# Kernel optimization log

Hardware: AMD Instinct MI355X
Metric: run time of the kernel (lower is better)

The kernel has to match this reference:

```python
import jax, jax.numpy as jnp
import numpy as np

KERNEL_MUL = 2.0
KERNEL_NUM = 5


def setup_inputs() -> dict:
    key = jax.random.key(0)
    k1, k2 = jax.random.split(key)
    source = jax.random.normal(k1, (4096, 256), dtype=jnp.float32)
    target = jax.random.normal(k2, (4096, 256), dtype=jnp.float32)
    return {"source": source, "target": target}


def _mmd(source, target):
    n = source.shape[0]
    m = target.shape[0]
    ns = n + m
    total = jnp.concatenate([source, target], axis=0)  # [ns, D]
    # Pairwise squared L2 distances without the O(ns^2 * D) broadcast tensor:
    # ||x_i - x_j||^2 = ||x_i||^2 + ||x_j||^2 - 2 <x_i, x_j>
    sq = jnp.sum(total * total, axis=1)  # [ns]
    l2 = sq[:, None] + sq[None, :] - 2.0 * (total @ total.T)  # [ns, ns]
    # bandwidth computed on detached data in the original (L2_distance.data)
    bandwidth = jax.lax.stop_gradient(jnp.sum(l2)) / (ns * ns - ns)
    bandwidth = bandwidth / (KERNEL_MUL ** (KERNEL_NUM // 2))
    # multi-bandwidth Gaussian kernel sum (fused single pass over l2)
    kernels = jnp.zeros_like(l2)
    for i in range(KERNEL_NUM):
        kernels = kernels + jnp.exp(-l2 / (bandwidth * KERNEL_MUL ** i))
    xx = jnp.sum(kernels[:n, :n]) / (n * n)
    xy = jnp.sum(kernels[:n, n:]) / (-n * m)
    yx = jnp.sum(kernels[n:, :n]) / (-m * n)
    yy = jnp.sum(kernels[n:, n:]) / (m * m)
    return xx + xy + yx + yy


def reference(source, target):
    return _mmd(source, target)
```

## Files before the change

### kernel.cpp

```cpp
#include <hip/hip_runtime.h>
#include <hip/hip_bf16.h>
#include <stdint.h>

#define NS 8192
#define NHALF 4096
#define DIM 256
#define BLK 128
#define BK 32
#define NKT (DIM / BK)
#define NTILES (NS / BLK)
#define HALF_TILES (NHALF / BLK)
#define NTRI (NTILES * (NTILES + 1) / 2)
#define PREP_BLOCKS 256

typedef __attribute__((ext_vector_type(8))) short bf16x8;
typedef __attribute__((ext_vector_type(4))) float f32x4;
typedef __attribute__((ext_vector_type(2))) float f32x2;
typedef __attribute__((ext_vector_type(8))) unsigned short u16x8;

#define XB_OFF   0
#define SQ_OFF   (NS * DIM * 2)
#define PART_OFF (SQ_OFF + NS * 4)
#define ACC_OFF  (PART_OFF + PREP_BLOCKS * DIM * 4)
#define C0_OFF   (ACC_OFF + 8)
#define WS_NEED  (C0_OFF + 16)

__device__ __forceinline__ unsigned short f2bf(float f) {
  unsigned int u = __float_as_uint(f);
  u += 0x7fffu + ((u >> 16) & 1u);
  return (unsigned short)(u >> 16);
}
__device__ __forceinline__ float bf2f(unsigned short h) {
  return __uint_as_float(((unsigned int)h) << 16);
}

__device__ __forceinline__ float fast_exp2(float x) {
#if __has_builtin(__builtin_amdgcn_exp2f)
  return __builtin_amdgcn_exp2f(x);
#else
  return exp2f(x);
#endif
}

__global__ __launch_bounds__(256) void mmd_prep(
    const float* __restrict__ src, const float* __restrict__ tgt,
    unsigned short* __restrict__ Xb, float* __restrict__ sq,
    float* __restrict__ partials, double* __restrict__ accK) {
  int tid = threadIdx.x;
  if (blockIdx.x == 0 && tid == 0) accK[0] = 0.0;
  int lane32 = tid & 31;
  int rgrp = tid >> 5;
  int c = lane32 * 8;
  int rowBase = blockIdx.x * 32;

  float colpart[8];
#pragma unroll
  for (int j = 0; j < 8; ++j) colpart[j] = 0.f;

#pragma unroll
  for (int p = 0; p < 4; ++p) {
    int row = rowBase + p * 8 + rgrp;
    const float* X = (row < NHALF) ? (src + (size_t)row * DIM)
                                   : (tgt + (size_t)(row - NHALF) * DIM);
    float4 v0 = *(const float4*)(X + c);
    float4 v1 = *(const float4*)(X + c + 4);
    float vals[8] = {v0.x, v0.y, v0.z, v0.w, v1.x, v1.y, v1.z, v1.w};
    u16x8 h;
    float s = 0.f;
#pragma unroll
    for (int j = 0; j < 8; ++j) {
      unsigned short b = f2bf(vals[j]);
      h[j] = b;
      float rb = bf2f(b);
      s += rb * rb;
      colpart[j] += rb;
    }
    *(u16x8*)(Xb + (size_t)row * DIM + c) = h;
    for (int o = 16; o > 0; o >>= 1) s += __shfl_down(s, o, 32);
    if (lane32 == 0) sq[row] = s;
  }

  __shared__ float cp[8][DIM];
  *(float4*)&cp[rgrp][c]     = make_float4(colpart[0], colpart[1], colpart[2], colpart[3]);
  *(float4*)&cp[rgrp][c + 4] = make_float4(colpart[4], colpart[5], colpart[6], colpart[7]);
  __syncthreads();
  float s8 = 0.f;
#pragma unroll
  for (int r = 0; r < 8; ++r) s8 += cp[r][tid];
  partials[blockIdx.x * DIM + tid] = s8;
}

__global__ __launch_bounds__(1024) void mmd_band(
    const float* __restrict__ partials, const float* __restrict__ sq,
    float* __restrict__ c0out) {
  __shared__ float CS[4][DIM];
  __shared__ float L1[1024];
  __shared__ double D2[DIM];
  int tid = threadIdx.x;
  int q = tid >> 8, col = tid & 255;
  float cs = 0.f;
  for (int b = 0; b < PREP_BLOCKS / 4; ++b)
    cs += partials[(q * 64 + b) * DIM + col];
  CS[q][col] = cs;
  const float4* s4 = (const float4*)sq;
  float4 va = s4[tid * 2], vb = s4[tid * 2 + 1];
  L1[tid] = (va.x + va.y + va.z + va.w) + (vb.x + vb.y + vb.z + vb.w);
  __syncthreads();
  if (tid < DIM) {
    float ctot = (CS[0][tid] + CS[1][tid]) + (CS[2][tid] + CS[3][tid]);
    D2[tid] = (double)ctot * (double)ctot;
    L1[tid] = (L1[tid] + L1[tid + 256]) + (L1[tid + 512] + L1[tid + 768]);
  }
  __syncthreads();
  for (int o = 128; o > 0; o >>= 1) {
    if (tid < o) { D2[tid] += D2[tid + o]; L1[tid] += L1[tid + o]; }
    __syncthreads();
  }
  if (tid == 0) {
    double S1 = (double)L1[0];
    double S2 = D2[0];
    double sum_l2 = 2.0 * (double)NS * S1 - 2.0 * S2;
    double bw = sum_l2 / ((double)NS * (double)NS - (double)NS);
    bw = bw / 4.0;
    c0out[0] = (float)(1.4426950408889634 / bw);
  }
}

#define STAGE(KT, BUF)                                                        \
  {                                                                           \
    _Pragma("unroll") for (int it = 0; it < 2; ++it) {                        \
      int idx = it * 256 + tid;                         \
      int r = idx >> 2, g = idx & 3;          \
      int gs = g ^ ((r >> 1) & 3);          \
      const unsigned short* ga =                                              \
          Xb + (size_t)(rowBase + r) * DIM + (KT)*BK + gs * 8;                \
      __builtin_amdgcn_global_load_lds(                                       \
          (const __attribute__((address_space(1))) void*)ga,                  \
          (__attribute__((address_space(3))) void*)(&As[BUF][idx * 8]), 16,   \
          0, 0);                                                              \
      const unsigned short* gb =                                              \
          Xb + (size_t)(colBase + r) * DIM + (KT)*BK + gs * 8;                \
      __builtin_amdgcn_global_load_lds(                                       \
          (const __attribute__((address_space(1))) void*)gb,                  \
          (__attribute__((address_space(3))) void*)(&Bs[BUF][idx * 8]), 16,   \
          0, 0);                                                              \
    }                                                                         \
  }

__global__ __launch_bounds__(256, 2) void mmd_gram(
    const unsigned short* __restrict__ Xb, const float* __restrict__ sq,
    const float* __restrict__ c0p, double* __restrict__ accK) {
  int l = blockIdx.x;
  int bj = (int)((sqrtf(8.f * (float)l + 1.f) - 1.f) * 0.5f);
  while ((bj + 1) * (bj + 2) / 2 <= l) bj++;
  while (bj * (bj + 1) / 2 > l) bj--;
  int bi = l - bj * (bj + 1) / 2;

  __shared__ __align__(16) unsigned short As[3][BLK * BK];
  __shared__ __align__(16) unsigned short Bs[3][BLK * BK];
  int tid = threadIdx.x;
  int wave = tid >> 6;
  int lane = tid & 63;
  int rowBase = bi * BLK, colBase = bj * BLK;
  int wr = (wave >> 1) * 64;
  int wc = (wave & 1) * 64;

  float c0v = *c0p;
  int r4 = (lane >> 4) * 4;
  f32x4 sqr4[4];
#pragma unroll
  for (int m = 0; m < 4; ++m)
    sqr4[m] = *(const f32x4*)&sq[rowBase + wr + m * 16 + r4];
  float sqc[4];
#pragma unroll
  for (int n = 0; n < 4; ++n)
    sqc[n] = sq[colBase + wc + n * 16 + (lane & 15)];

  f32x4 acc[4][4];
#pragma unroll
  for (int m = 0; m < 4; ++m)
#pragma unroll
    for (int n = 0; n < 4; ++n) acc[m][n] = (f32x4){0.f, 0.f, 0.f, 0.f};

  STAGE(0, 0);
  STAGE(1, 1);

#pragma unroll
  for (int kt = 0; kt < NKT; ++kt) {
    int cur = kt % 3;
    if (kt == NKT - 1)
      asm volatile("s_waitcnt vmcnt(0)" ::: "memory");
    else
      asm volatile("s_waitcnt vmcnt(4)" ::: "memory");
    __builtin_amdgcn_s_barrier();
    __builtin_amdgcn_sched_barrier(0);

    bf16x8 af[4], bfr[4];
    int kg = lane >> 4;
#pragma unroll
    for (int m = 0; m < 4; ++m) {
      int r = wr + m * 16 + (lane & 15);
      af[m] = *(const bf16x8*)(&As[cur][r * BK + (kg ^ ((r >> 1) & 3)) * 8]);
    }
#pragma unroll
    for (int n = 0; n < 4; ++n) {
      int r = wc + n * 16 + (lane & 15);
      bfr[n] = *(const bf16x8*)(&Bs[cur][r * BK + (kg ^ ((r >> 1) & 3)) * 8]);
    }

    if (kt < NKT - 2) STAGE(kt + 2, (kt + 2) % 3);

#pragma unroll
    for (int m = 0; m < 4; ++m)
#pragma unroll
      for (int n = 0; n < 4; ++n)
        acc[m][n] = __builtin_amdgcn_mfma_f32_16x16x32_bf16(
            af[m], bfr[n], acc[m][n], 0, 0, 0);
  }

  float cE = -0.0625f * c0v;
  float t2 = -2.f * cE;
  f32x2 t2v = (f32x2){t2, t2};
  f32x2 aP[4][2];
#pragma unroll
  for (int m = 0; m < 4; ++m)
#pragma unroll
    for (int p = 0; p < 2; ++p)
      aP[m][p] = (f32x2){cE * sqr4[m][p * 2], cE * sqr4[m][p * 2 + 1]};
  f32x2 ts = (f32x2){0.f, 0.f};
#pragma unroll
  for (int m = 0; m < 4; ++m)
#pragma unroll
    for (int n = 0; n < 4; ++n) {
      f32x2 bv = (f32x2){cE * sqc[n], cE * sqc[n]};
#pragma unroll
      for (int p = 0; p < 2; ++p) {
        f32x2 a2 = (f32x2){acc[m][n][p * 2], acc[m][n][p * 2 + 1]};
        f32x2 arg = a2 * t2v + (aP[m][p] + bv);
        f32x2 e4;
        e4.x = fast_exp2(arg.x);
        e4.y = fast_exp2(arg.y);
        f32x2 e3 = e4 * e4;
        f32x2 e2 = e3 * e3;
        f32x2 e1 = e2 * e2;
        f32x2 e0 = e1 * e1;
        ts += ((e4 + e3) + (e2 + e1)) + e0;
      }
    }
  float tsum = ts.x + ts.y;

  float* red4 = (float*)&As[0][0];
#pragma unroll
  for (int o = 32; o > 0; o >>= 1) tsum += __shfl_down(tsum, o);
  if (lane == 0) red4[wave] = tsum;
  __syncthreads();
  if (tid == 0) {
    float t = (red4[0] + red4[1]) + (red4[2] + red4[3]);
    float sign = ((bi < HALF_TILES) == (bj < HALF_TILES)) ? 1.f : -1.f;
    float factor = (bi == bj) ? sign : 2.f * sign;
    atomicAdd(accK, (double)(factor * t));
  }
}

__global__ void mmd_final(const double* __restrict__ accK, float* __restrict__ out) {
  out[0] = (float)(accK[0] / ((double)NHALF * (double)NHALF));
}

extern "C" void kernel_launch(void* const* d_in, const int* in_sizes, int n_in,
                              void* d_out, int out_size, void* d_ws, size_t ws_size,
                              hipStream_t stream) {
  if (ws_size < (size_t)WS_NEED) return;
  const float* src = (const float*)d_in[0];
  const float* tgt = (const float*)d_in[1];
  char* ws = (char*)d_ws;
  unsigned short* Xb = (unsigned short*)(ws + XB_OFF);
  float* sq          = (float*)(ws + SQ_OFF);
  float* partials    = (float*)(ws + PART_OFF);
  double* accK       = (double*)(ws + ACC_OFF);
  float* c0          = (float*)(ws + C0_OFF);

  mmd_prep<<<PREP_BLOCKS, 256, 0, stream>>>(src, tgt, Xb, sq, partials, accK);
  mmd_band<<<1, 1024, 0, stream>>>(partials, sq, c0);
  mmd_gram<<<NTRI, 256, 0, stream>>>(Xb, sq, c0, accK);
  mmd_final<<<1, 1, 0, stream>>>(accK, (float*)d_out);
}
```

Baseline: 56.37 us.

## Eliminate bandwidth reduction kernel via atomics and recompute bandwidth per gram block

The separate single-block bandwidth kernel is removed. The prep kernel now atomically accumulates column sums and the total squared-norm sum into zeroed workspace, and every gram block recomputes the bandwidth from those 256 column sums with a wave reduction. Gram block indices are remapped with a stride-8 interleave, and the next-stage global-to-LDS prefetch is issued before the LDS fragment reads. This drops one serial launch and its tail latency, at the cost of a memset launch, float atomics whose summation order is nondeterministic, and redundant per-block bandwidth math.

Result: slower. 93.02 us (+65.0%).

```diff
diff --git a/kernel.cpp b/kernel.cpp
--- a/kernel.cpp
+++ b/kernel.cpp
@@ -20,10 +20,11 @@
 
 #define XB_OFF   0
 #define SQ_OFF   (NS * DIM * 2)
-#define PART_OFF (SQ_OFF + NS * 4)
-#define ACC_OFF  (PART_OFF + PREP_BLOCKS * DIM * 4)
-#define C0_OFF   (ACC_OFF + 8)
-#define WS_NEED  (C0_OFF + 16)
+#define ACC_OFF  (SQ_OFF + NS * 4)
+#define S1_OFF   (ACC_OFF + 8)
+#define CS_OFF   (ACC_OFF + 16)
+#define ZERO_BYTES (16 + DIM * 4)
+#define WS_NEED  (CS_OFF + DIM * 4)
 
 __device__ __forceinline__ unsigned short f2bf(float f) {
   unsigned int u = __float_as_uint(f);
@@ -45,9 +46,8 @@
 __global__ __launch_bounds__(256) void mmd_prep(
     const float* __restrict__ src, const float* __restrict__ tgt,
     unsigned short* __restrict__ Xb, float* __restrict__ sq,
-    float* __restrict__ partials, double* __restrict__ accK) {
+    float* __restrict__ colsum, float* __restrict__ S1p) {
   int tid = threadIdx.x;
-  if (blockIdx.x == 0 && tid == 0) accK[0] = 0.0;
   int lane32 = tid & 31;
   int rgrp = tid >> 5;
   int c = lane32 * 8;
@@ -56,6 +56,7 @@
   float colpart[8];
 #pragma unroll
   for (int j = 0; j < 8; ++j) colpart[j] = 0.f;
+  float ssum = 0.f;
 
 #pragma unroll
   for (int p = 0; p < 4; ++p) {
@@ -77,52 +78,24 @@
     }
     *(u16x8*)(Xb + (size_t)row * DIM + c) = h;
     for (int o = 16; o > 0; o >>= 1) s += __shfl_down(s, o, 32);
-    if (lane32 == 0) sq[row] = s;
+    if (lane32 == 0) { sq[row] = s; ssum += s; }
   }
 
   __shared__ float cp[8][DIM];
+  __shared__ float rowsum[8];
   *(float4*)&cp[rgrp][c]     = make_float4(colpart[0], colpart[1], colpart[2], colpart[3]);
   *(float4*)&cp[rgrp][c + 4] = make_float4(colpart[4], colpart[5], colpart[6], colpart[7]);
+  if (lane32 == 0) rowsum[rgrp] = ssum;
   __syncthreads();
   float s8 = 0.f;
 #pragma unroll
   for (int r = 0; r < 8; ++r) s8 += cp[r][tid];
-  partials[blockIdx.x * DIM + tid] = s8;
-}
-
-__global__ __launch_bounds__(1024) void mmd_band(
-    const float* __restrict__ partials, const float* __restrict__ sq,
-    float* __restrict__ c0out) {
-  __shared__ float CS[4][DIM];
-  __shared__ float L1[1024];
-  __shared__ double D2[DIM];
-  int tid = threadIdx.x;
-  int q = tid >> 8, col = tid & 255;
-  float cs = 0.f;
-  for (int b = 0; b < PREP_BLOCKS / 4; ++b)
-    cs += partials[(q * 64 + b) * DIM + col];
-  CS[q][col] = cs;
-  const float4* s4 = (const float4*)sq;
-  float4 va = s4[tid * 2], vb = s4[tid * 2 + 1];
-  L1[tid] = (va.x + va.y + va.z + va.w) + (vb.x + vb.y + vb.z + vb.w);
-  __syncthreads();
-  if (tid < DIM) {
-    float ctot = (CS[0][tid] + CS[1][tid]) + (CS[2][tid] + CS[3][tid]);
-    D2[tid] = (double)ctot * (double)ctot;
-    L1[tid] = (L1[tid] + L1[tid + 256]) + (L1[tid + 512] + L1[tid + 768]);
-  }
-  __syncthreads();
-  for (int o = 128; o > 0; o >>= 1) {
-    if (tid < o) { D2[tid] += D2[tid + o]; L1[tid] += L1[tid + o]; }
-    __syncthreads();
-  }
+  atomicAdd(&colsum[tid], s8);
   if (tid == 0) {
-    double S1 = (double)L1[0];
-    double S2 = D2[0];
-    double sum_l2 = 2.0 * (double)NS * S1 - 2.0 * S2;
-    double bw = sum_l2 / ((double)NS * (double)NS - (double)NS);
-    bw = bw / 4.0;
-    c0out[0] = (float)(1.4426950408889634 / bw);
+    float t = 0.f;
+#pragma unroll
+    for (int r = 0; r < 8; ++r) t += rowsum[r];
+    atomicAdd(S1p, t);
   }
 }
 
@@ -149,8 +122,10 @@
 
 __global__ __launch_bounds__(256, 2) void mmd_gram(
     const unsigned short* __restrict__ Xb, const float* __restrict__ sq,
-    const float* __restrict__ c0p, double* __restrict__ accK) {
-  int l = blockIdx.x;
+    const float* __restrict__ colsum, const float* __restrict__ S1p,
+    double* __restrict__ accK) {
+  int bid = blockIdx.x;
+  int l = (bid & 7) * (NTRI / 8) + (bid >> 3);
   int bj = (int)((sqrtf(8.f * (float)l + 1.f) - 1.f) * 0.5f);
   while ((bj + 1) * (bj + 2) / 2 <= l) bj++;
   while (bj * (bj + 1) / 2 > l) bj--;
@@ -165,7 +140,10 @@
   int wr = (wave >> 1) * 64;
   int wc = (wave & 1) * 64;
 
-  float c0v = *c0p;
+  float csv[4];
+#pragma unroll
+  for (int i = 0; i < 4; ++i) csv[i] = colsum[i * 64 + lane];
+  float S1v = *S1p;
   int r4 = (lane >> 4) * 4;
   f32x4 sqr4[4];
 #pragma unroll
@@ -195,6 +173,8 @@
     __builtin_amdgcn_s_barrier();
     __builtin_amdgcn_sched_barrier(0);
 
+    if (kt < NKT - 2) STAGE(kt + 2, (kt + 2) % 3);
+
     bf16x8 af[4], bfr[4];
     int kg = lane >> 4;
 #pragma unroll
@@ -208,8 +188,6 @@
       bfr[n] = *(const bf16x8*)(&Bs[cur][r * BK + (kg ^ ((r >> 1) & 3)) * 8]);
     }
 
-    if (kt < NKT - 2) STAGE(kt + 2, (kt + 2) % 3);
-
 #pragma unroll
     for (int m = 0; m < 4; ++m)
 #pragma unroll
@@ -218,8 +196,16 @@
             af[m], bfr[n], acc[m][n], 0, 0, 0);
   }
 
-  float cE = -0.0625f * c0v;
+  float s2p = 0.f;
+#pragma unroll
+  for (int i = 0; i < 4; ++i) s2p += csv[i] * csv[i];
+#pragma unroll
+  for (int o = 32; o > 0; o >>= 1) s2p += __shfl_xor(s2p, o);
+  double sum_l2 = 2.0 * (double)NS * (double)S1v - 2.0 * (double)s2p;
+  double bw = sum_l2 / ((double)NS * (double)NS - (double)NS) * 0.25;
+  float cE = (float)(-1.4426950408889634 * 0.0625 / bw);
   float t2 = -2.f * cE;
+
   f32x2 t2v = (f32x2){t2, t2};
   f32x2 aP[4][2];
 #pragma unroll
@@ -275,12 +261,12 @@
   char* ws = (char*)d_ws;
   unsigned short* Xb = (unsigned short*)(ws + XB_OFF);
   float* sq          = (float*)(ws + SQ_OFF);
-  float* partials    = (float*)(ws + PART_OFF);
   double* accK       = (double*)(ws + ACC_OFF);
-  float* c0          = (float*)(ws + C0_OFF);
-
-  mmd_prep<<<PREP_BLOCKS, 256, 0, stream>>>(src, tgt, Xb, sq, partials, accK);
-  mmd_band<<<1, 1024, 0, stream>>>(partials, sq, c0);
-  mmd_gram<<<NTRI, 256, 0, stream>>>(Xb, sq, c0, accK);
+  float* S1p         = (float*)(ws + S1_OFF);
+  float* colsum      = (float*)(ws + CS_OFF);
+
+  hipMemsetAsync(ws + ACC_OFF, 0, ZERO_BYTES, stream);
+  mmd_prep<<<PREP_BLOCKS, 256, 0, stream>>>(src, tgt, Xb, sq, colsum, S1p);
+  mmd_gram<<<NTRI, 256, 0, stream>>>(Xb, sq, colsum, S1p, accK);
   mmd_final<<<1, 1, 0, stream>>>(accK, (float*)d_out);
 }
```

## Load MFMA fragments directly from global memory, dropping LDS staging

Applied to the files above, without the earlier changes.

Removes the triple-buffered LDS staging (global_load_lds plus barriers) in the Gram kernel. Each wave now loads its bf16 A/B fragments straight from global memory into registers for every K step. It also moves the squared-norm and bandwidth loads after the MMA loop. This removes LDS traffic and block-level synchronization, and frees shared memory for higher occupancy. In exchange, rows shared between waves are fetched redundantly from global or L2, and the software pipelining that hid load latency is lost.

New measurement: 89.22 us. +58.3%, slower.

```diff
diff --git a/kernel.cpp b/kernel.cpp
--- a/kernel.cpp
+++ b/kernel.cpp
@@ -126,27 +126,6 @@
   }
 }
 
-#define STAGE(KT, BUF)                                                        \
-  {                                                                           \
-    _Pragma("unroll") for (int it = 0; it < 2; ++it) {                        \
-      int idx = it * 256 + tid;                         \
-      int r = idx >> 2, g = idx & 3;          \
-      int gs = g ^ ((r >> 1) & 3);          \
-      const unsigned short* ga =                                              \
-          Xb + (size_t)(rowBase + r) * DIM + (KT)*BK + gs * 8;                \
-      __builtin_amdgcn_global_load_lds(                                       \
-          (const __attribute__((address_space(1))) void*)ga,                  \
-          (__attribute__((address_space(3))) void*)(&As[BUF][idx * 8]), 16,   \
-          0, 0);                                                              \
-      const unsigned short* gb =                                              \
-          Xb + (size_t)(colBase + r) * DIM + (KT)*BK + gs * 8;                \
-      __builtin_amdgcn_global_load_lds(                                       \
-          (const __attribute__((address_space(1))) void*)gb,                  \
-          (__attribute__((address_space(3))) void*)(&Bs[BUF][idx * 8]), 16,   \
-          0, 0);                                                              \
-    }                                                                         \
-  }
-
 __global__ __launch_bounds__(256, 2) void mmd_gram(
     const unsigned short* __restrict__ Xb, const float* __restrict__ sq,
     const float* __restrict__ c0p, double* __restrict__ accK) {
@@ -156,25 +135,20 @@
   while (bj * (bj + 1) / 2 > l) bj--;
   int bi = l - bj * (bj + 1) / 2;
 
-  __shared__ __align__(16) unsigned short As[3][BLK * BK];
-  __shared__ __align__(16) unsigned short Bs[3][BLK * BK];
+  __shared__ float red4[4];
   int tid = threadIdx.x;
   int wave = tid >> 6;
   int lane = tid & 63;
   int rowBase = bi * BLK, colBase = bj * BLK;
   int wr = (wave >> 1) * 64;
   int wc = (wave & 1) * 64;
-
-  float c0v = *c0p;
-  int r4 = (lane >> 4) * 4;
-  f32x4 sqr4[4];
-#pragma unroll
-  for (int m = 0; m < 4; ++m)
-    sqr4[m] = *(const f32x4*)&sq[rowBase + wr + m * 16 + r4];
-  float sqc[4];
-#pragma unroll
-  for (int n = 0; n < 4; ++n)
-    sqc[n] = sq[colBase + wc + n * 16 + (lane & 15)];
+  int lane15 = lane & 15;
+  int kg = lane >> 4;
+
+  const unsigned short* pA =
+      Xb + (size_t)(rowBase + wr + lane15) * DIM + kg * 8;
+  const unsigned short* pB =
+      Xb + (size_t)(colBase + wc + lane15) * DIM + kg * 8;
 
   f32x4 acc[4][4];
 #pragma unroll
@@ -182,34 +156,15 @@
 #pragma unroll
     for (int n = 0; n < 4; ++n) acc[m][n] = (f32x4){0.f, 0.f, 0.f, 0.f};
 
-  STAGE(0, 0);
-  STAGE(1, 1);
-
 #pragma unroll
   for (int kt = 0; kt < NKT; ++kt) {
-    int cur = kt % 3;
-    if (kt == NKT - 1)
-      asm volatile("s_waitcnt vmcnt(0)" ::: "memory");
-    else
-      asm volatile("s_waitcnt vmcnt(4)" ::: "memory");
-    __builtin_amdgcn_s_barrier();
-    __builtin_amdgcn_sched_barrier(0);
-
     bf16x8 af[4], bfr[4];
-    int kg = lane >> 4;
-#pragma unroll
-    for (int m = 0; m < 4; ++m) {
-      int r = wr + m * 16 + (lane & 15);
-      af[m] = *(const bf16x8*)(&As[cur][r * BK + (kg ^ ((r >> 1) & 3)) * 8]);
-    }
-#pragma unroll
-    for (int n = 0; n < 4; ++n) {
-      int r = wc + n * 16 + (lane & 15);
-      bfr[n] = *(const bf16x8*)(&Bs[cur][r * BK + (kg ^ ((r >> 1) & 3)) * 8]);
-    }
-
-    if (kt < NKT - 2) STAGE(kt + 2, (kt + 2) % 3);
-
+#pragma unroll
+    for (int m = 0; m < 4; ++m)
+      af[m] = *(const bf16x8*)(pA + (size_t)m * 16 * DIM + kt * BK);
+#pragma unroll
+    for (int n = 0; n < 4; ++n)
+      bfr[n] = *(const bf16x8*)(pB + (size_t)n * 16 * DIM + kt * BK);
 #pragma unroll
     for (int m = 0; m < 4; ++m)
 #pragma unroll
@@ -217,6 +172,17 @@
         acc[m][n] = __builtin_amdgcn_mfma_f32_16x16x32_bf16(
             af[m], bfr[n], acc[m][n], 0, 0, 0);
   }
+
+  float c0v = *c0p;
+  int r4 = kg * 4;
+  f32x4 sqr4[4];
+#pragma unroll
+  for (int m = 0; m < 4; ++m)
+    sqr4[m] = *(const f32x4*)&sq[rowBase + wr + m * 16 + r4];
+  float sqc[4];
+#pragma unroll
+  for (int n = 0; n < 4; ++n)
+    sqc[n] = sq[colBase + wc + n * 16 + lane15];
 
   float cE = -0.0625f * c0v;
   float t2 = -2.f * cE;
@@ -249,7 +215,6 @@
     }
   float tsum = ts.x + ts.y;
 
-  float* red4 = (float*)&As[0][0];
 #pragma unroll
   for (int o = 32; o > 0; o >>= 1) tsum += __shfl_down(tsum, o);
   if (lane == 0) red4[wave] = tsum;
```
